# Kernel tuning notes

Hardware: AMD Instinct MI355X
Metric: run time of the kernel (lower is better)

The kernel has to match this reference:

```python
import jax, jax.numpy as jnp
import numpy as np

N = 40000
IN_DIM = 128
HID = 64
E = 640000


def sage_conv(x, edge_index, W_l, b_l, W_r):
    """PyG SAGEConv with mean aggregation.
    out = lin_l(mean_{j in N(i)} x_j) + lin_r(x_i)
    edge_index[0]=src (message source), edge_index[1]=dst (aggregation target).
    """
    src, dst = edge_index[0], edge_index[1]
    n = x.shape[0]
    msgs = x[src]                                            # [E, d] gather
    sums = jax.ops.segment_sum(msgs, dst, num_segments=n)    # [N, d]
    cnt = jax.ops.segment_sum(jnp.ones((msgs.shape[0],), x.dtype), dst,
                              num_segments=n)                # [N]
    mean = sums / jnp.maximum(cnt, 1.0)[:, None]
    return mean @ W_l.T + b_l + x @ W_r.T


def setup_inputs() -> dict:
    key = jax.random.key(0)
    ks = jax.random.split(key, 8)
    x = jax.random.normal(ks[0], (N, IN_DIM), dtype=jnp.float32)
    edge_index = jax.random.randint(ks[1], (2, E), 0, N, dtype=jnp.int32)
    s1 = 1.0 / np.sqrt(IN_DIM)
    s2 = 1.0 / np.sqrt(HID)
    W1_l = jax.random.uniform(ks[2], (HID, IN_DIM), jnp.float32, -s1, s1)
    b1_l = jax.random.uniform(ks[3], (HID,), jnp.float32, -s1, s1)
    W1_r = jax.random.uniform(ks[4], (HID, IN_DIM), jnp.float32, -s1, s1)
    W2_l = jax.random.uniform(ks[5], (HID, HID), jnp.float32, -s2, s2)
    b2_l = jax.random.uniform(ks[6], (HID,), jnp.float32, -s2, s2)
    W2_r = jax.random.uniform(ks[7], (HID, HID), jnp.float32, -s2, s2)
    return {"x": x, "edge_index": edge_index,
            "W1_l": W1_l, "b1_l": b1_l, "W1_r": W1_r,
            "W2_l": W2_l, "b2_l": b2_l, "W2_r": W2_r}


def reference(x, edge_index, W1_l, b1_l, W1_r, W2_l, b2_l, W2_r):
    h = sage_conv(x, edge_index, W1_l, b1_l, W1_r)
    h = jax.nn.relu(h)
    # dropout is identity in eval mode (reference baseline is deterministic)
    z = sage_conv(h, edge_index, W2_l, b2_l, W2_r)
    return z
```

## Files before the change

kernel.cpp:

```cpp
#include <hip/hip_runtime.h>

#define INDIM 128
#define HID 64
#define CAP 64
#define GEMM_BLOCKS 625
#define BIN_BLOCKS 256
#define PREP_BLOCKS 32
#define RSH 7
#define RMASK ((1 << RSH) - 1)
#define NRANGE 313
#define SBCAP 28

__device__ __forceinline__ float bf2f(unsigned short u) {
    union { unsigned int i; float f; } c; c.i = ((unsigned int)u) << 16; return c.f;
}
__device__ __forceinline__ unsigned short f2bf(float f) {
    union { float f; unsigned int i; } c; c.f = f;
    return (unsigned short)((c.i + 0x7FFFu + ((c.i >> 16) & 1u)) >> 16);
}

__device__ __forceinline__ void agg2n(const unsigned short* __restrict__ T,
                                      int idxA, int idxB, int degA, int degB,
                                      int q, int f4,
                                      float aA[4], float aB[4]) {
    const int ncA = (degA + 3) >> 2, ncB = (degB + 3) >> 2;
    const int ncM = ncA > ncB ? ncA : ncB;
    for (int c = 0; c < ncM; c += 4) {
        #pragma unroll
        for (int u = 0; u < 4; ++u) {
            const int lanesel = (c + u) * 4 + q;
            int sA = __shfl(idxA, lanesel, 64);
            int sB = __shfl(idxB, lanesel, 64);
            const bool lA = lanesel < degA;
            const bool lB = lanesel < degB;
            sA = lA ? sA : 0;
            sB = lB ? sB : 0;
            const uint2 vA = *(const uint2*)&T[(size_t)sA * 64 + f4 * 4];
            const uint2 vB = *(const uint2*)&T[(size_t)sB * 64 + f4 * 4];
            const float mA = lA ? 1.f : 0.f;
            const float mB = lB ? 1.f : 0.f;
            aA[0] += bf2f((unsigned short)(vA.x & 0xffffu)) * mA;
            aA[1] += bf2f((unsigned short)(vA.x >> 16)) * mA;
            aA[2] += bf2f((unsigned short)(vA.y & 0xffffu)) * mA;
            aA[3] += bf2f((unsigned short)(vA.y >> 16)) * mA;
            aB[0] += bf2f((unsigned short)(vB.x & 0xffffu)) * mB;
            aB[1] += bf2f((unsigned short)(vB.x >> 16)) * mB;
            aB[2] += bf2f((unsigned short)(vB.y & 0xffffu)) * mB;
            aB[3] += bf2f((unsigned short)(vB.y >> 16)) * mB;
        }
    }
    #pragma unroll
    for (int j = 0; j < 4; ++j) {
        aA[j] += __shfl_xor(aA[j], 16, 64);
        aA[j] += __shfl_xor(aA[j], 32, 64);
        aB[j] += __shfl_xor(aB[j], 16, 64);
        aB[j] += __shfl_xor(aB[j], 32, 64);
    }
}


__global__ __launch_bounds__(256) void k_bin_prep(
    const int* __restrict__ src, const int* __restrict__ dst,
    unsigned int* __restrict__ hist_global, unsigned int* __restrict__ ebin,
    const float* __restrict__ W1l, const float* __restrict__ W1r,
    const float* __restrict__ W2l, const float* __restrict__ W2r,
    float* __restrict__ WT1l, float* __restrict__ WT1r,
    float* __restrict__ WT2l, float* __restrict__ WT2r, int E) {
    const int tid = threadIdx.x;

    if (blockIdx.x >= BIN_BLOCKS) {
        const int gtid = (blockIdx.x - BIN_BLOCKS) * 256 + tid;
        if (gtid < 64 * 128) {
            int j = gtid >> 7, k = gtid & 127;
            WT1l[k * 64 + j] = W1l[gtid];
            WT1r[k * 64 + j] = W1r[gtid];
        }
        if (gtid < 64 * 64) {
            int j = gtid >> 6, k = gtid & 63;
            WT2l[k * 64 + j] = W2l[gtid];
            WT2r[k * 64 + j] = W2r[gtid];
        }
        return;
    }

    __shared__ unsigned int hist[NRANGE];
    __shared__ unsigned int cur[NRANGE];
    const int b = blockIdx.x;
    const int ech = (E + BIN_BLOCKS - 1) / BIN_BLOCKS;
    const int e0 = b * ech;
    const int e1 = (e0 + ech < E) ? e0 + ech : E;

    for (int r = tid; r < NRANGE; r += 256) { hist[r] = 0; cur[r] = 0; }
    __syncthreads();
    for (int e = e0 + tid; e < e1; e += 256)
        atomicAdd(&hist[((unsigned)dst[e]) >> RSH], 1u);
    __syncthreads();
    for (int r = tid; r < NRANGE; r += 256)
        hist_global[(size_t)r * BIN_BLOCKS + b] = hist[r];
    __syncthreads();
    for (int e = e0 + tid; e < e1; e += 256) {
        const unsigned d = (unsigned)dst[e];
        const unsigned s = (unsigned)src[e];
        const unsigned r = d >> RSH;
        const unsigned off = atomicAdd(&cur[r], 1u);
        if (off < SBCAP)
            ebin[((size_t)r * BIN_BLOCKS + b) * SBCAP + off] = (d << 16) | s;
    }
}


__global__ __launch_bounds__(256) void k_gemm1_place(
    const float* __restrict__ A,
    const float* __restrict__ WTl, const float* __restrict__ WTr,
    unsigned short* __restrict__ Pb, float* __restrict__ Q,
    const unsigned int* __restrict__ hist_global,
    const unsigned int* __restrict__ ebin,
    int* __restrict__ cnt, unsigned short* __restrict__ sorted, int N) {
    __shared__ float As[64][INDIM + 1];
    __shared__ unsigned int lcnt[1 << RSH];
    const int tid = threadIdx.x;

    if (blockIdx.x < NRANGE) {
        const int r = blockIdx.x;
        if (tid < (1 << RSH)) lcnt[tid] = 0;
        __syncthreads();
        const int lane = tid & 63, w = tid >> 6;
        const int sb_local = lane >> 3, ent0 = lane & 7;
        for (int g = w * 8; g < BIN_BLOCKS; g += 32) {
            const int sb = g + sb_local;
            unsigned c = hist_global[(size_t)r * BIN_BLOCKS + sb];
            if (c > SBCAP) c = SBCAP;
            const unsigned int* eb = ebin + ((size_t)r * BIN_BLOCKS + sb) * SBCAP;
            for (unsigned p = 0; p * 8 < c; ++p) {
                const unsigned e = p * 8 + ent0;
                if (e < c) {
                    const unsigned pkt = eb[e];
                    const unsigned d = pkt >> 16;
                    const unsigned slot = atomicAdd(&lcnt[d & RMASK], 1u);
                    if (slot < CAP)
                        sorted[(d << 6) + slot] = (unsigned short)(pkt & 0xffffu);
                }
            }
        }
        __syncthreads();
        for (int l = tid; l < (1 << RSH); l += 256) {
            const int node = (r << RSH) + l;
            if (node < N) cnt[node] = (int)lcnt[l];
        }
        return;
    }

    const int bm = (blockIdx.x - NRANGE) * 64;
    for (int idx = tid; idx < 64 * 32; idx += 256) {
        int row = idx >> 5, kq = idx & 31;
        const float4 v = ((const float4*)A)[(size_t)(bm + row) * 32 + kq];
        As[row][kq * 4 + 0] = v.x; As[row][kq * 4 + 1] = v.y;
        As[row][kq * 4 + 2] = v.z; As[row][kq * 4 + 3] = v.w;
    }
    __syncthreads();

    const int tx = tid & 15, ty = tid >> 4;
    const int n0 = ty * 4;
    float accl[4][4] = {}, accr[4][4] = {};
    #pragma unroll 8
    for (int k = 0; k < INDIM; ++k) {
        float a[4];
        #pragma unroll
        for (int i = 0; i < 4; ++i) a[i] = As[n0 + i][k];
        const float4 blv = ((const float4*)WTl)[k * 16 + tx];
        const float4 brv = ((const float4*)WTr)[k * 16 + tx];
        const float bl[4] = {blv.x, blv.y, blv.z, blv.w};
        const float br[4] = {brv.x, brv.y, brv.z, brv.w};
        #pragma unroll
        for (int i = 0; i < 4; ++i) {
            #pragma unroll
            for (int j = 0; j < 4; ++j) {
                accl[i][j] += a[i] * bl[j];
                accr[i][j] += a[i] * br[j];
            }
        }
    }
    #pragma unroll
    for (int i = 0; i < 4; ++i) {
        int m = bm + n0 + i;
        ushort4 pv;
        pv.x = f2bf(accl[i][0]); pv.y = f2bf(accl[i][1]);
        pv.z = f2bf(accl[i][2]); pv.w = f2bf(accl[i][3]);
        ((ushort4*)Pb)[(size_t)m * 16 + tx] = pv;
        ((float4*)Q)[(size_t)m * 16 + tx] =
            make_float4(accr[i][0], accr[i][1], accr[i][2], accr[i][3]);
    }
}


__global__ __launch_bounds__(256) void k_agg1(
    const unsigned short* __restrict__ Pb, const float* __restrict__ Q,
    const float* __restrict__ b1,
    const int* __restrict__ cnt, const unsigned short* __restrict__ sorted,
    unsigned short* __restrict__ Hb, float* __restrict__ H, int N) {
    const int wave = (blockIdx.x * 256 + threadIdx.x) >> 6;
    const int lane = threadIdx.x & 63;
    const int q = lane >> 4, f4 = lane & 15;
    const int nA = wave * 2, nB = nA + 1;
    if (nA >= N) return;
    int dv = (lane < 2 && nA + lane < N) ? cnt[nA + lane] : 0;
    int degA = __shfl(dv, 0, 64); degA = degA > CAP ? CAP : degA;
    int degB = __shfl(dv, 1, 64); degB = degB > CAP ? CAP : degB;
    const int idxA = (int)sorted[(nA << 6) + lane];
    const int idxB = (nB < N) ? (int)sorted[(nB << 6) + lane] : 0;
    float aA[4] = {}, aB[4] = {};
    agg2n(Pb, idxA, idxB, degA, degB, q, f4, aA, aB);

    const int node = (q == 0) ? nA : nB;
    const float* ap = (q == 0) ? aA : aB;
    const int deg = (q == 0) ? degA : degB;
    if ((q == 0 || q == 1) && node < N) {
        const float inv = 1.0f / fmaxf((float)deg, 1.0f);
        const float4 qv = *(const float4*)&Q[(size_t)node * 64 + f4 * 4];
        const float4 bv = *(const float4*)&b1[f4 * 4];
        const float h0 = fmaxf(ap[0] * inv + bv.x + qv.x, 0.f);
        const float h1 = fmaxf(ap[1] * inv + bv.y + qv.y, 0.f);
        const float h2 = fmaxf(ap[2] * inv + bv.z + qv.z, 0.f);
        const float h3 = fmaxf(ap[3] * inv + bv.w + qv.w, 0.f);
        uint2 u;
        u.x = (unsigned)f2bf(h0) | ((unsigned)f2bf(h1) << 16);
        u.y = (unsigned)f2bf(h2) | ((unsigned)f2bf(h3) << 16);
        *(uint2*)&Hb[(size_t)node * 64 + f4 * 4] = u;
        *(float4*)&H[(size_t)node * 64 + f4 * 4] = make_float4(h0, h1, h2, h3);
    }
}


__global__ __launch_bounds__(256) void k_agg2h(
    const unsigned short* __restrict__ Hb,
    const int* __restrict__ cnt, const unsigned short* __restrict__ sorted,
    float* __restrict__ meanH, int N) {
    const int wave = (blockIdx.x * 256 + threadIdx.x) >> 6;
    const int lane = threadIdx.x & 63;
    const int q = lane >> 4, f4 = lane & 15;
    const int nA = wave * 2, nB = nA + 1;
    if (nA >= N) return;
    int dv = (lane < 2 && nA + lane < N) ? cnt[nA + lane] : 0;
    int degA = __shfl(dv, 0, 64); degA = degA > CAP ? CAP : degA;
    int degB = __shfl(dv, 1, 64); degB = degB > CAP ? CAP : degB;
    const int idxA = (int)sorted[(nA << 6) + lane];
    const int idxB = (nB < N) ? (int)sorted[(nB << 6) + lane] : 0;
    float aA[4] = {}, aB[4] = {};
    agg2n(Hb, idxA, idxB, degA, degB, q, f4, aA, aB);

    const int node = (q == 0) ? nA : nB;
    const float* ap = (q == 0) ? aA : aB;
    const int deg = (q == 0) ? degA : degB;
    if ((q == 0 || q == 1) && node < N) {
        const float inv = 1.0f / fmaxf((float)deg, 1.0f);
        *(float4*)&meanH[(size_t)node * 64 + f4 * 4] =
            make_float4(ap[0] * inv, ap[1] * inv, ap[2] * inv, ap[3] * inv);
    }
}


__global__ __launch_bounds__(256) void k_gemm_z(
    const float* __restrict__ meanH, const float* __restrict__ H,
    const float* __restrict__ WTl, const float* __restrict__ WTr,
    const float* __restrict__ b2, float* __restrict__ z, int N) {
    __shared__ float As1[64][HID + 1];
    __shared__ float As2[64][HID + 1];
    const int tid = threadIdx.x;
    const int bm = blockIdx.x * 64;
    for (int idx = tid; idx < 64 * 16; idx += 256) {
        int row = idx >> 4, kq = idx & 15;
        const float4 v1 = ((const float4*)meanH)[(size_t)(bm + row) * 16 + kq];
        const float4 v2 = ((const float4*)H)[(size_t)(bm + row) * 16 + kq];
        As1[row][kq * 4 + 0] = v1.x; As1[row][kq * 4 + 1] = v1.y;
        As1[row][kq * 4 + 2] = v1.z; As1[row][kq * 4 + 3] = v1.w;
        As2[row][kq * 4 + 0] = v2.x; As2[row][kq * 4 + 1] = v2.y;
        As2[row][kq * 4 + 2] = v2.z; As2[row][kq * 4 + 3] = v2.w;
    }
    __syncthreads();

    const int tx = tid & 15, ty = tid >> 4;
    const int n0 = ty * 4;
    float acc[4][4] = {};
    #pragma unroll 8
    for (int k = 0; k < HID; ++k) {
        float a1[4], a2[4];
        #pragma unroll
        for (int i = 0; i < 4; ++i) { a1[i] = As1[n0 + i][k]; a2[i] = As2[n0 + i][k]; }
        const float4 blv = ((const float4*)WTl)[k * 16 + tx];
        const float4 brv = ((const float4*)WTr)[k * 16 + tx];
        const float bl[4] = {blv.x, blv.y, blv.z, blv.w};
        const float br[4] = {brv.x, brv.y, brv.z, brv.w};
        #pragma unroll
        for (int i = 0; i < 4; ++i) {
            #pragma unroll
            for (int j = 0; j < 4; ++j)
                acc[i][j] += a1[i] * bl[j] + a2[i] * br[j];
        }
    }
    const float4 bv = *(const float4*)&b2[tx * 4];
    #pragma unroll
    for (int i = 0; i < 4; ++i) {
        int m = bm + n0 + i;
        if (m < N) {
            ((float4*)z)[(size_t)m * 16 + tx] =
                make_float4(acc[i][0] + bv.x, acc[i][1] + bv.y,
                            acc[i][2] + bv.z, acc[i][3] + bv.w);
        }
    }
}


extern "C" void kernel_launch(void* const* d_in, const int* in_sizes, int n_in,
                              void* d_out, int out_size, void* d_ws, size_t ws_size,
                              hipStream_t stream) {
    const float* x   = (const float*)d_in[0];
    const int*  edge = (const int*)d_in[1];
    const float* W1l = (const float*)d_in[2];
    const float* b1l = (const float*)d_in[3];
    const float* W1r = (const float*)d_in[4];
    const float* W2l = (const float*)d_in[5];
    const float* b2l = (const float*)d_in[6];
    const float* W2r = (const float*)d_in[7];

    const int N = in_sizes[0] / INDIM;
    const int E = in_sizes[1] / 2;
    const int* src = edge;
    const int* dst = edge + E;

    char* w = (char*)d_ws;
    auto carve = [&](size_t bytes) {
        char* p = w; w += (bytes + 255) & ~(size_t)255; return p;
    };
    unsigned short* Pb  = (unsigned short*)carve((size_t)N * 64 * 2);
    unsigned short* Hb  = (unsigned short*)carve((size_t)N * 64 * 2);
    float* Q     = (float*)carve((size_t)N * 64 * 4);
    float* H     = (float*)carve((size_t)N * 64 * 4);
    float* meanH = (float*)carve((size_t)N * 64 * 4);
    float* WT1l = (float*)carve(128 * 64 * 4);
    float* WT1r = (float*)carve(128 * 64 * 4);
    float* WT2l = (float*)carve(64 * 64 * 4);
    float* WT2r = (float*)carve(64 * 64 * 4);
    int* cnt    = (int*)carve((size_t)N * 4);
    unsigned short* sorted = (unsigned short*)carve((size_t)N * CAP * 2);
    unsigned int* hist_global = (unsigned int*)carve((size_t)NRANGE * BIN_BLOCKS * 4);
    unsigned int* ebin = (unsigned int*)carve((size_t)NRANGE * BIN_BLOCKS * SBCAP * 4);

    float* zout = (float*)d_out;

    const int gT = (N + 63) / 64;
    const int nwave = (N + 1) / 2;
    const int gW2 = (nwave + 3) / 4;

    k_bin_prep<<<BIN_BLOCKS + PREP_BLOCKS, 256, 0, stream>>>(
        src, dst, hist_global, ebin,
        W1l, W1r, W2l, W2r, WT1l, WT1r, WT2l, WT2r, E);
    k_gemm1_place<<<NRANGE + GEMM_BLOCKS, 256, 0, stream>>>(
        x, WT1l, WT1r, Pb, Q, hist_global, ebin, cnt, sorted, N);
    k_agg1<<<gW2, 256, 0, stream>>>(Pb, Q, b1l, cnt, sorted, Hb, H, N);
    k_agg2h<<<gW2, 256, 0, stream>>>(Hb, cnt, sorted, meanH, N);
    k_gemm_z<<<gT, 256, 0, stream>>>(meanH, H, WT2l, WT2r, b2l, zout, N);
}
```

Measured before the change: 102.9 us.

## Split bf16 feature tables into two half-width planes and aggregate per half

Stores the bf16 projected features and hidden features as two separate 32-column planes and runs each aggregation kernel twice, once per half. Each gather pass then touches a 2.5 MB table instead of a 5 MB one, aiming to keep the random-access working set resident in L2/LLC. The cost is extra launches, re-reading indices and counts twice, and narrower 4-byte gather loads per lane.

```diff
diff --git a/kernel.cpp b/kernel.cpp
--- a/kernel.cpp
+++ b/kernel.cpp
@@ -19,10 +19,10 @@
     return (unsigned short)((c.i + 0x7FFFu + ((c.i >> 16) & 1u)) >> 16);
 }
 
-__device__ __forceinline__ void agg2n(const unsigned short* __restrict__ T,
+__device__ __forceinline__ void agg2p(const unsigned short* __restrict__ T,
                                       int idxA, int idxB, int degA, int degB,
                                       int q, int f4,
-                                      float aA[4], float aB[4]) {
+                                      float aA[2], float aB[2]) {
     const int ncA = (degA + 3) >> 2, ncB = (degB + 3) >> 2;
     const int ncM = ncA > ncB ? ncA : ncB;
     for (int c = 0; c < ncM; c += 4) {
@@ -35,22 +35,18 @@
             const bool lB = lanesel < degB;
             sA = lA ? sA : 0;
             sB = lB ? sB : 0;
-            const uint2 vA = *(const uint2*)&T[(size_t)sA * 64 + f4 * 4];
-            const uint2 vB = *(const uint2*)&T[(size_t)sB * 64 + f4 * 4];
+            const unsigned vA = *(const unsigned*)&T[(size_t)sA * 32 + f4 * 2];
+            const unsigned vB = *(const unsigned*)&T[(size_t)sB * 32 + f4 * 2];
             const float mA = lA ? 1.f : 0.f;
             const float mB = lB ? 1.f : 0.f;
-            aA[0] += bf2f((unsigned short)(vA.x & 0xffffu)) * mA;
-            aA[1] += bf2f((unsigned short)(vA.x >> 16)) * mA;
-            aA[2] += bf2f((unsigned short)(vA.y & 0xffffu)) * mA;
-            aA[3] += bf2f((unsigned short)(vA.y >> 16)) * mA;
-            aB[0] += bf2f((unsigned short)(vB.x & 0xffffu)) * mB;
-            aB[1] += bf2f((unsigned short)(vB.x >> 16)) * mB;
-            aB[2] += bf2f((unsigned short)(vB.y & 0xffffu)) * mB;
-            aB[3] += bf2f((unsigned short)(vB.y >> 16)) * mB;
+            aA[0] += bf2f((unsigned short)(vA & 0xffffu)) * mA;
+            aA[1] += bf2f((unsigned short)(vA >> 16)) * mA;
+            aB[0] += bf2f((unsigned short)(vB & 0xffffu)) * mB;
+            aB[1] += bf2f((unsigned short)(vB >> 16)) * mB;
         }
     }
     #pragma unroll
-    for (int j = 0; j < 4; ++j) {
+    for (int j = 0; j < 2; ++j) {
         aA[j] += __shfl_xor(aA[j], 16, 64);
         aA[j] += __shfl_xor(aA[j], 32, 64);
         aB[j] += __shfl_xor(aB[j], 16, 64);
@@ -112,7 +108,8 @@
 __global__ __launch_bounds__(256) void k_gemm1_place(
     const float* __restrict__ A,
     const float* __restrict__ WTl, const float* __restrict__ WTr,
-    unsigned short* __restrict__ Pb, float* __restrict__ Q,
+    unsigned short* __restrict__ PbL, unsigned short* __restrict__ PbH,
+    float* __restrict__ Q,
     const unsigned int* __restrict__ hist_global,
     const unsigned int* __restrict__ ebin,
     int* __restrict__ cnt, unsigned short* __restrict__ sorted, int N) {
@@ -186,18 +183,21 @@
         ushort4 pv;
         pv.x = f2bf(accl[i][0]); pv.y = f2bf(accl[i][1]);
         pv.z = f2bf(accl[i][2]); pv.w = f2bf(accl[i][3]);
-        ((ushort4*)Pb)[(size_t)m * 16 + tx] = pv;
+        if (tx < 8) ((ushort4*)PbL)[(size_t)m * 8 + tx] = pv;
+        else        ((ushort4*)PbH)[(size_t)m * 8 + (tx - 8)] = pv;
         ((float4*)Q)[(size_t)m * 16 + tx] =
             make_float4(accr[i][0], accr[i][1], accr[i][2], accr[i][3]);
     }
 }
 
 
-__global__ __launch_bounds__(256) void k_agg1(
-    const unsigned short* __restrict__ Pb, const float* __restrict__ Q,
-    const float* __restrict__ b1,
+__global__ __launch_bounds__(256) void k_agg1P(
+    const unsigned short* __restrict__ T,
+    const float* __restrict__ Q, const float* __restrict__ b1,
     const int* __restrict__ cnt, const unsigned short* __restrict__ sorted,
-    unsigned short* __restrict__ Hb, float* __restrict__ H, int N) {
+    unsigned short* __restrict__ HbP,
+    float* __restrict__ H,
+    int poff, int N) {
     const int wave = (blockIdx.x * 256 + threadIdx.x) >> 6;
     const int lane = threadIdx.x & 63;
     const int q = lane >> 4, f4 = lane & 15;
@@ -208,33 +208,29 @@
     int degB = __shfl(dv, 1, 64); degB = degB > CAP ? CAP : degB;
     const int idxA = (int)sorted[(nA << 6) + lane];
     const int idxB = (nB < N) ? (int)sorted[(nB << 6) + lane] : 0;
-    float aA[4] = {}, aB[4] = {};
-    agg2n(Pb, idxA, idxB, degA, degB, q, f4, aA, aB);
+    float aA[2] = {}, aB[2] = {};
+    agg2p(T, idxA, idxB, degA, degB, q, f4, aA, aB);
 
     const int node = (q == 0) ? nA : nB;
     const float* ap = (q == 0) ? aA : aB;
     const int deg = (q == 0) ? degA : degB;
     if ((q == 0 || q == 1) && node < N) {
         const float inv = 1.0f / fmaxf((float)deg, 1.0f);
-        const float4 qv = *(const float4*)&Q[(size_t)node * 64 + f4 * 4];
-        const float4 bv = *(const float4*)&b1[f4 * 4];
+        const float2 qv = *(const float2*)&Q[(size_t)node * 64 + poff + f4 * 2];
+        const float2 bv = *(const float2*)&b1[poff + f4 * 2];
         const float h0 = fmaxf(ap[0] * inv + bv.x + qv.x, 0.f);
         const float h1 = fmaxf(ap[1] * inv + bv.y + qv.y, 0.f);
-        const float h2 = fmaxf(ap[2] * inv + bv.z + qv.z, 0.f);
-        const float h3 = fmaxf(ap[3] * inv + bv.w + qv.w, 0.f);
-        uint2 u;
-        u.x = (unsigned)f2bf(h0) | ((unsigned)f2bf(h1) << 16);
-        u.y = (unsigned)f2bf(h2) | ((unsigned)f2bf(h3) << 16);
-        *(uint2*)&Hb[(size_t)node * 64 + f4 * 4] = u;
-        *(float4*)&H[(size_t)node * 64 + f4 * 4] = make_float4(h0, h1, h2, h3);
-    }
-}
-
-
-__global__ __launch_bounds__(256) void k_agg2h(
-    const unsigned short* __restrict__ Hb,
+        *(unsigned*)&HbP[(size_t)node * 32 + f4 * 2] =
+            (unsigned)f2bf(h0) | ((unsigned)f2bf(h1) << 16);
+        *(float2*)&H[(size_t)node * 64 + poff + f4 * 2] = make_float2(h0, h1);
+    }
+}
+
+
+__global__ __launch_bounds__(256) void k_agg2P(
+    const unsigned short* __restrict__ T,
     const int* __restrict__ cnt, const unsigned short* __restrict__ sorted,
-    float* __restrict__ meanH, int N) {
+    float* __restrict__ meanH, int poff, int N) {
     const int wave = (blockIdx.x * 256 + threadIdx.x) >> 6;
     const int lane = threadIdx.x & 63;
     const int q = lane >> 4, f4 = lane & 15;
@@ -245,16 +241,16 @@
     int degB = __shfl(dv, 1, 64); degB = degB > CAP ? CAP : degB;
     const int idxA = (int)sorted[(nA << 6) + lane];
     const int idxB = (nB < N) ? (int)sorted[(nB << 6) + lane] : 0;
-    float aA[4] = {}, aB[4] = {};
-    agg2n(Hb, idxA, idxB, degA, degB, q, f4, aA, aB);
+    float aA[2] = {}, aB[2] = {};
+    agg2p(T, idxA, idxB, degA, degB, q, f4, aA, aB);
 
     const int node = (q == 0) ? nA : nB;
     const float* ap = (q == 0) ? aA : aB;
     const int deg = (q == 0) ? degA : degB;
     if ((q == 0 || q == 1) && node < N) {
         const float inv = 1.0f / fmaxf((float)deg, 1.0f);
-        *(float4*)&meanH[(size_t)node * 64 + f4 * 4] =
-            make_float4(ap[0] * inv, ap[1] * inv, ap[2] * inv, ap[3] * inv);
+        *(float2*)&meanH[(size_t)node * 64 + poff + f4 * 2] =
+            make_float2(ap[0] * inv, ap[1] * inv);
     }
 }
 
@@ -331,8 +327,10 @@
     auto carve = [&](size_t bytes) {
         char* p = w; w += (bytes + 255) & ~(size_t)255; return p;
     };
-    unsigned short* Pb  = (unsigned short*)carve((size_t)N * 64 * 2);
-    unsigned short* Hb  = (unsigned short*)carve((size_t)N * 64 * 2);
+    unsigned short* PbL = (unsigned short*)carve((size_t)N * 32 * 2);
+    unsigned short* PbH = (unsigned short*)carve((size_t)N * 32 * 2);
+    unsigned short* HbL = (unsigned short*)carve((size_t)N * 32 * 2);
+    unsigned short* HbH = (unsigned short*)carve((size_t)N * 32 * 2);
     float* Q     = (float*)carve((size_t)N * 64 * 4);
     float* H     = (float*)carve((size_t)N * 64 * 4);
     float* meanH = (float*)carve((size_t)N * 64 * 4);
@@ -355,8 +353,10 @@
         src, dst, hist_global, ebin,
         W1l, W1r, W2l, W2r, WT1l, WT1r, WT2l, WT2r, E);
     k_gemm1_place<<<NRANGE + GEMM_BLOCKS, 256, 0, stream>>>(
-        x, WT1l, WT1r, Pb, Q, hist_global, ebin, cnt, sorted, N);
-    k_agg1<<<gW2, 256, 0, stream>>>(Pb, Q, b1l, cnt, sorted, Hb, H, N);
-    k_agg2h<<<gW2, 256, 0, stream>>>(Hb, cnt, sorted, meanH, N);
+        x, WT1l, WT1r, PbL, PbH, Q, hist_global, ebin, cnt, sorted, N);
+    k_agg1P<<<gW2, 256, 0, stream>>>(PbL, Q, b1l, cnt, sorted, HbL, H, 0, N);
+    k_agg1P<<<gW2, 256, 0, stream>>>(PbH, Q, b1l, cnt, sorted, HbH, H, 32, N);
+    k_agg2P<<<gW2, 256, 0, stream>>>(HbL, cnt, sorted, meanH, 0, N);
+    k_agg2P<<<gW2, 256, 0, stream>>>(HbH, cnt, sorted, meanH, 32, N);
     k_gemm_z<<<gT, 256, 0, stream>>>(meanH, H, WT2l, WT2r, b2l, zout, N);
 }
```

After: 133.3 us. 1.3x slower.
